# Kernel optimization log

Hardware: AMD Instinct MI355X
Metric: run time of the kernel (lower is better)

## Reference

```python
import jax, jax.numpy as jnp
import numpy as np

RANGES = {"measure": 256, "beat": 16, "position": 128, "duration": 128, "pitch": 256,
          "instrument": 129, "velocity": 128, "key_sign": 24, "time_sign": 48, "tempo": 49}
R_TOTAL = sum(RANGES.values())  # 1162
NUMERATORS = jnp.array([1, 2, 3, 4, 5, 6, 7, 8, 9, 10, 12, 16], dtype=jnp.int32)
TOT_NUM = 12
NEG = jnp.float32(-1e9)


def _prefix_gather(x, axis=1):
    # value at position i becomes the cumulative value at index min(i+1, S-1):
    # reproduces the tf mask `range(S) <= idx+1` (prefix up to i+1 inclusive).
    S = x.shape[axis]
    idx = jnp.minimum(jnp.arange(S) + 1, S - 1)
    return jnp.take(x, idx, axis=axis)


def _present_mask(song, dtype_id, feat, R):
    # occ[b,i,v] = True iff some token j<=i+1 has type dtype_id and song[b,j,feat]==v
    # (vectorized form of tensor_scatter_nd_max over a prefix, via one-hot + cummax)
    match = song[..., 0] == dtype_id                       # [B,S]
    onehot = (song[..., feat][..., None] == jnp.arange(R)) & match[..., None]
    cum = jax.lax.cummax(onehot.astype(jnp.int32), axis=1)
    return _prefix_gather(cum, 1).astype(bool)             # [B,S,R]


def _has_any(song, dtype_id):
    match = (song[..., 0] == dtype_id).astype(jnp.int32)
    return _prefix_gather(jax.lax.cummax(match, axis=1), 1).astype(bool)  # [B,S]


def _last_value(song, dtype_id, feat):
    # song[b, argmax_j(match*j) , feat] over the prefix j<=i+1; tf argmax of all
    # zeros returns 0, reproduced by where(match, j, 0) + cummax.
    match = song[..., 0] == dtype_id
    j = jnp.arange(song.shape[1])
    last_idx = _prefix_gather(jax.lax.cummax(jnp.where(match, j, 0), axis=1), 1)
    return jnp.take_along_axis(song[..., feat], last_idx, axis=1)  # [B,S]


def _forward(song, chosen_type, scores):
    B, S, _ = song.shape
    Rm, Rb = RANGES["measure"], RANGES["beat"]
    ar_m = jnp.arange(RANGES["measure"]); ar_b = jnp.arange(RANGES["beat"])
    ar_p = jnp.arange(RANGES["position"])
    ar_ks = jnp.arange(RANGES["key_sign"]); ar_ts = jnp.arange(RANGES["time_sign"])
    ar_tp = jnp.arange(RANGES["tempo"])
    t = chosen_type[..., None]  # [B,S,1]

    inst_present = _present_mask(song, 1, 6, RANGES["instrument"])  # [B,S,129]
    has_inst = inst_present.any(-1, keepdims=True)

    last_ks = _last_value(song, 4, 8);  oh_ks = last_ks[..., None] == ar_ks
    last_ts = _last_value(song, 5, 9);  oh_ts = last_ts[..., None] == ar_ts
    last_tp = _last_value(song, 6, 10); oh_tp = last_tp[..., None] == ar_tp
    has_ks = _has_any(song, 4)[..., None]
    has_ts = _has_any(song, 5)[..., None]

    # ---- chosen_type == 3 (note-like token) ----
    min_measure = song[..., 1]
    pred_m = jnp.argmax(scores[..., :Rm], axis=-1).astype(jnp.int32)
    c1 = pred_m == min_measure
    min_beat = jnp.where(c1, song[..., 2], 0)
    pred_b = jnp.argmax(scores[..., Rm:Rm + Rb], axis=-1).astype(jnp.int32)
    c2 = c1 & (pred_b == min_beat)
    min_pos = jnp.where(c2, song[..., 3], 0)
    max_beat = NUMERATORS[jnp.mod(last_ts, TOT_NUM)]  # get_max_beat_from_time_sign
    m3 = ar_m >= min_measure[..., None]
    b3 = (ar_b >= min_beat[..., None]) & (ar_b < max_beat[..., None])
    p3 = ar_p >= min_pos[..., None]

    # ---- chosen_type == 1 (instrument): forbid already-present instruments ----
    inst1 = jnp.where(has_inst, ~inst_present, True)

    # ---- chosen_type in 4..6 (key_sign / time_sign / tempo) ----
    min_m46 = jnp.where((song[..., 2] == 0) & (song[..., 3] == 0),
                        song[..., 1], song[..., 1] + 1)
    m46 = ar_m >= min_m46[..., None]
    ks4 = jnp.where(has_ks, ~oh_ks, True)
    ts5 = jnp.where(has_ts, ~oh_ts, True)
    tp6 = ~oh_tp

    is3 = t == 3
    measure_mask = jnp.where(is3, m3, jnp.where((t >= 4) & (t <= 6), m46, True))
    beat_mask = jnp.where(is3, b3, True)
    position_mask = jnp.where(is3, p3, True)
    duration_mask = jnp.ones((B, S, RANGES["duration"]), bool)
    pitch_mask = jnp.ones((B, S, RANGES["pitch"]), bool)
    instrument_mask = jnp.where(is3, inst_present, jnp.where(t == 1, inst1, True))
    velocity_mask = jnp.ones((B, S, RANGES["velocity"]), bool)
    key_sign_mask = jnp.where(is3, oh_ks, jnp.where(t == 4, ks4, True))
    time_sign_mask = jnp.where(is3, oh_ts, jnp.where(t == 5, ts5, True))
    tempo_mask = jnp.where(is3, oh_tp, jnp.where(t == 6, tp6, True))

    mask = jnp.concatenate([measure_mask, beat_mask, position_mask, duration_mask,
                            pitch_mask, instrument_mask, velocity_mask,
                            key_sign_mask, time_sign_mask, tempo_mask], axis=-1)
    return jnp.where(mask, scores, NEG)  # masked logits [B,S,R_TOTAL]


def setup_inputs() -> dict:
    key = jax.random.key(0)
    k_song, k_type, k_scores = jax.random.split(key, 3)
    B, S = 8, 2047  # SEQ_LEN-1 with SEQ_LEN=2048
    col_max = [8, RANGES["measure"], RANGES["beat"], RANGES["position"],
               RANGES["duration"], RANGES["pitch"], RANGES["instrument"],
               RANGES["velocity"], RANGES["key_sign"], RANGES["time_sign"],
               RANGES["tempo"]]
    kcols = jax.random.split(k_song, 11)
    song = jnp.stack([jax.random.randint(kcols[c], (B, S), 0, col_max[c],
                                         dtype=jnp.int32) for c in range(11)], axis=-1)
    chosen_type = jax.random.randint(k_type, (B, S), 0, 8, dtype=jnp.int32)
    scores = jax.random.normal(k_scores, (B, S, R_TOTAL), dtype=jnp.float32)
    return {"song": song, "chosen_type": chosen_type, "scores": scores}


def reference(song, chosen_type, scores):
    return _forward(song, chosen_type, scores)
```

## Files before the change

kernel.cpp:

```cpp
#include <hip/hip_runtime.h>
#include <cstdint>
#include <cstddef>

#define S_LEN 2047
#define BATCH 8
#define R_TOT 1162
#define NCHUNK 8
#define NEGV (-1e9f)

#define CARRY_OFF 393024

__device__ __constant__ int d_numerators[12] = {1, 2, 3, 4, 5, 6, 7, 8, 9, 10, 12, 16};

__global__ __launch_bounds__(256) void scan_local(const int* __restrict__ song,
                                                  unsigned* __restrict__ local) {
    const int b = blockIdx.x >> 3;
    const int c = blockIdx.x & 7;
    const int tid = threadIdx.x;
    const int j = c * 256 + tid;
    __shared__ unsigned lds_f[3][256];
    __shared__ unsigned lds_inst[5][256];
    const unsigned HAS = 1u << 16;
    const long base = (long)b * S_LEN;

    unsigned e_f[3] = {0, 0, 0};
    unsigned e_inst[5] = {0, 0, 0, 0, 0};
    if (j < S_LEN) {
        const int* rj = song + (base + j) * 11;
        const int type = rj[0];
        if (type == 4)      e_f[0] = HAS | (unsigned)rj[8];
        else if (type == 5) e_f[1] = HAS | (unsigned)rj[9];
        else if (type == 6) e_f[2] = HAS | (unsigned)rj[10];
        else if (type == 1) { const int v = rj[6]; e_inst[v >> 5] = 1u << (v & 31); }
    }
#pragma unroll
    for (int w = 0; w < 3; w++) lds_f[w][tid] = e_f[w];
#pragma unroll
    for (int w = 0; w < 5; w++) lds_inst[w][tid] = e_inst[w];
    __syncthreads();

    for (int off = 1; off < 256; off <<= 1) {
        unsigned p_f[3] = {0, 0, 0};
        unsigned p_inst[5] = {0, 0, 0, 0, 0};
        if (tid >= off) {
#pragma unroll
            for (int w = 0; w < 3; w++) p_f[w] = lds_f[w][tid - off];
#pragma unroll
            for (int w = 0; w < 5; w++) p_inst[w] = lds_inst[w][tid - off];
        }
        __syncthreads();
        if (tid >= off) {
#pragma unroll
            for (int w = 0; w < 3; w++) {
                if (!(e_f[w] & HAS)) e_f[w] = p_f[w];
                lds_f[w][tid] = e_f[w];
            }
#pragma unroll
            for (int w = 0; w < 5; w++) {
                e_inst[w] |= p_inst[w];
                lds_inst[w][tid] = e_inst[w];
            }
        }
        __syncthreads();
    }

    if (j < S_LEN) {
        const unsigned w0 =
            (e_f[0] & 0xFFu) | ((e_f[1] & 0xFFu) << 8) | ((e_f[2] & 0xFFu) << 16) |
            (((e_f[0] >> 16) & 1u) << 24) | (((e_f[1] >> 16) & 1u) << 25) |
            (((e_f[2] >> 16) & 1u) << 26);
        unsigned* sp = local + (size_t)(base + j) * 6;
        sp[0] = w0;
#pragma unroll
        for (int w = 0; w < 5; w++) sp[1 + w] = e_inst[w];
    }
}

__global__ __launch_bounds__(64) void scan_carry(const int* __restrict__ song,
                                                 const unsigned* __restrict__ local,
                                                 unsigned* __restrict__ carry) {
    const int b = threadIdx.x;
    if (b >= BATCH) return;
    const int* r0 = song + (size_t)b * S_LEN * 11;
    unsigned cks = (unsigned)r0[8], cts = (unsigned)r0[9], ctp = (unsigned)r0[10];
    unsigned chas = 0;
    unsigned cinst[5] = {0, 0, 0, 0, 0};
    for (int c = 0; c < NCHUNK; c++) {
        unsigned* cp = carry + ((size_t)b * NCHUNK + c) * 6;
        cp[0] = (cks & 0xFFu) | ((cts & 0xFFu) << 8) | ((ctp & 0xFFu) << 16) | (chas << 24);
#pragma unroll
        for (int w = 0; w < 5; w++) cp[1 + w] = cinst[w];
        const int pos = min((c + 1) * 256, S_LEN) - 1;
        const unsigned* lp = local + ((size_t)b * S_LEN + pos) * 6;
        const unsigned a0 = lp[0];
        if ((a0 >> 24) & 1u) cks = a0 & 0xFFu;
        if ((a0 >> 25) & 1u) cts = (a0 >> 8) & 0xFFu;
        if ((a0 >> 26) & 1u) ctp = (a0 >> 16) & 0xFFu;
        chas |= (a0 >> 24) & 7u;
#pragma unroll
        for (int w = 0; w < 5; w++) cinst[w] |= lp[1 + w];
    }
}

__global__ __launch_bounds__(256) void mask_kernel(const int* __restrict__ song,
                                                   const int* __restrict__ ctype,
                                                   const float* __restrict__ scores,
                                                   const unsigned* __restrict__ local,
                                                   const unsigned* __restrict__ carry,
                                                   float* __restrict__ out) {
    const int row = blockIdx.x;
    const int tid = threadIdx.x;
    const int b = row / S_LEN;
    const int i = row - b * S_LEN;

    __shared__ float s_val[128];
    __shared__ int   s_idx[128];
    __shared__ float sb_val[8];
    __shared__ int   sb_idx[8];
    __shared__ int   s_info[10];
    __shared__ int   f_info[17];

    const size_t rbase = (size_t)row * R_TOT;
    const float2* s2 = (const float2*)(scores + rbase);
    float2* o2 = (float2*)(out + rbase);

    const int t0 = ctype[row];

    const float2 r0 = s2[tid];
    const float2 r1 = s2[tid + 256];
    float2 r2 = make_float2(0.f, 0.f);
    if (tid < 69) r2 = s2[tid + 512];

    if (t0 == 0 || t0 == 2 || t0 == 7) {
        o2[tid] = r0;
        o2[tid + 256] = r1;
        if (tid < 69) o2[tid + 512] = r2;
        return;
    }

    if (tid < 128) {
        const bool sec = (r0.y > r0.x);
        s_val[tid] = sec ? r0.y : r0.x;
        s_idx[tid] = 2 * tid + (sec ? 1 : 0);
    } else if (tid < 136) {
        const bool sec = (r0.y > r0.x);
        sb_val[tid - 128] = sec ? r0.y : r0.x;
        sb_idx[tid - 128] = (2 * tid - 256) + (sec ? 1 : 0);
    } else if (tid < 142) {
        const int w = tid - 136;
        const int e = min(i + 1, S_LEN - 1);
        const unsigned lw = local[((size_t)b * S_LEN + e) * 6 + w];
        const unsigned cw = carry[((size_t)b * NCHUNK + (e >> 8)) * 6 + w];
        unsigned v;
        if (w == 0) {
            const unsigned ks = ((lw >> 24) & 1u) ? (lw & 0xFFu) : (cw & 0xFFu);
            const unsigned ts = ((lw >> 25) & 1u) ? ((lw >> 8) & 0xFFu) : ((cw >> 8) & 0xFFu);
            const unsigned tp = ((lw >> 26) & 1u) ? ((lw >> 16) & 0xFFu) : ((cw >> 16) & 0xFFu);
            const unsigned hks = ((lw >> 24) | (cw >> 24)) & 1u;
            const unsigned hts = ((lw >> 25) | (cw >> 25)) & 1u;
            v = ks | (ts << 8) | (tp << 16) | (hks << 24) | (hts << 25);
        } else {
            v = lw | cw;
        }
        s_info[w] = (int)v;
    } else if (tid < 146) {
        const int* srow = song + (size_t)row * 11;
        if (tid == 142) s_info[6] = srow[1];
        if (tid == 143) s_info[7] = srow[2];
        if (tid == 144) s_info[8] = srow[3];
        if (tid == 145) s_info[9] = ctype[row];
    }
    __syncthreads();

    if (t0 == 3) {
        for (int s = 64; s > 0; s >>= 1) {
            if (tid < s) {
                if (s_val[tid + s] > s_val[tid]) {
                    s_val[tid] = s_val[tid + s];
                    s_idx[tid] = s_idx[tid + s];
                }
            }
            __syncthreads();
        }
    }

    if (tid == 0) {
        int pred_m = -1, pred_b = -1;
        if (t0 == 3) {
            pred_m = s_idx[0];
            float bv = sb_val[0];
            pred_b = sb_idx[0];
#pragma unroll
            for (int q = 1; q < 8; q++) {
                if (sb_val[q] > bv) { bv = sb_val[q]; pred_b = sb_idx[q]; }
            }
        }
        const unsigned pack = (unsigned)s_info[0];
        const int song1 = s_info[6], song2 = s_info[7], song3 = s_info[8];
        const int t = s_info[9];
        const bool c1 = (pred_m == song1);
        const int min_beat = c1 ? song2 : 0;
        const bool c2 = c1 && (pred_b == min_beat);
        const int min_pos = c2 ? song3 : 0;
        const int last_ks = pack & 0xFF;
        const int last_ts = (pack >> 8) & 0xFF;
        const int last_tp = (pack >> 16) & 0xFF;
        f_info[0] = t;
        f_info[1] = song1;
        f_info[2] = min_beat;
        f_info[3] = min_pos;
        f_info[4] = (song2 == 0 && song3 == 0) ? song1 : song1 + 1;
        f_info[5] = d_numerators[last_ts % 12];
        f_info[6] = last_ks;
        f_info[7] = last_ts;
        f_info[8] = last_tp;
        f_info[9]  = (int)((pack >> 24) & 1u);
        f_info[10] = (int)((pack >> 25) & 1u);
        const unsigned u = (unsigned)s_info[1] | (unsigned)s_info[2] | (unsigned)s_info[3] |
                           (unsigned)s_info[4] | (unsigned)s_info[5];
        f_info[11] = (u != 0u);
        f_info[12] = s_info[1]; f_info[13] = s_info[2]; f_info[14] = s_info[3];
        f_info[15] = s_info[4]; f_info[16] = s_info[5];
    }
    __syncthreads();

    const int t = f_info[0];
    const int min_measure = f_info[1], min_beat = f_info[2], min_pos = f_info[3];
    const int min_m46 = f_info[4], max_beat = f_info[5];
    const int last_ks = f_info[6], last_ts = f_info[7], last_tp = f_info[8];
    const bool has_ks = f_info[9] != 0, has_ts = f_info[10] != 0, has_inst = f_info[11] != 0;
    unsigned inst[5];
#pragma unroll
    for (int w = 0; w < 5; w++) inst[w] = (unsigned)f_info[12 + w];
    const bool is3 = (t == 3);
    const bool is46 = (t >= 4) && (t <= 6);

    auto maskf = [&](int col) -> bool {
        if (col < 256) {
            if (is3) return col >= min_measure;
            if (is46) return col >= min_m46;
            return true;
        } else if (col < 272) {
            if (!is3) return true;
            const int v = col - 256;
            return (v >= min_beat) && (v < max_beat);
        } else if (col < 400) {
            return is3 ? ((col - 272) >= min_pos) : true;
        } else if (col < 784) {
            return true;
        } else if (col < 913) {
            const int v = col - 784;
            const bool pres = ((inst[v >> 5] >> (v & 31)) & 1u) != 0u;
            if (is3) return pres;
            if (t == 1) return has_inst ? !pres : true;
            return true;
        } else if (col < 1041) {
            return true;
        } else if (col < 1065) {
            const int v = col - 1041;
            if (is3) return v == last_ks;
            if (t == 4) return has_ks ? (v != last_ks) : true;
            return true;
        } else if (col < 1113) {
            const int v = col - 1065;
            if (is3) return v == last_ts;
            if (t == 5) return has_ts ? (v != last_ts) : true;
            return true;
        } else {
            const int v = col - 1113;
            if (is3) return v == last_tp;
            if (t == 6) return v != last_tp;
            return true;
        }
    };

    float2 w;
    int c = 2 * tid;
    w.x = maskf(c)     ? r0.x : NEGV;
    w.y = maskf(c + 1) ? r0.y : NEGV;
    o2[tid] = w;

    c = 512 + 2 * tid;
    w.x = maskf(c)     ? r1.x : NEGV;
    w.y = maskf(c + 1) ? r1.y : NEGV;
    o2[tid + 256] = w;

    if (tid < 69) {
        c = 1024 + 2 * tid;
        w.x = maskf(c)     ? r2.x : NEGV;
        w.y = maskf(c + 1) ? r2.y : NEGV;
        o2[tid + 512] = w;
    }
}

extern "C" void kernel_launch(void* const* d_in, const int* in_sizes, int n_in,
                              void* d_out, int out_size, void* d_ws, size_t ws_size,
                              hipStream_t stream) {
    const int* song = (const int*)d_in[0];
    const int* ctype = (const int*)d_in[1];
    const float* scores = (const float*)d_in[2];
    float* out = (float*)d_out;
    unsigned* local = (unsigned*)d_ws;
    unsigned* carry = (unsigned*)((char*)d_ws + CARRY_OFF);

    scan_local<<<BATCH * NCHUNK, 256, 0, stream>>>(song, local);
    scan_carry<<<1, 64, 0, stream>>>(song, local, carry);
    mask_kernel<<<BATCH * S_LEN, 256, 0, stream>>>(song, ctype, scores, local, carry, out);
}
```

Before: 146.7 us.

## Split masking into per-row bitmask kernel and flat float4 streaming kernel

The single per-row mask kernel becomes two kernels. A row_state kernel computes a 37-word per-row bitmask into workspace, reading scores only for type-3 rows. A grid-stride stream_mask kernel then applies that bitmask to the whole scores tensor with coalesced float4 loads and stores. The goal is to replace the awkward 1162-wide per-row float2 access with a uniform streaming pass. The cost is an extra kernel launch, a bitmask write and read, and per-element division and gathers into the bitmask table. If the workspace is too small, the old kernel is used instead.

Result: slower. 172.2 us (+17.4%).

```diff
diff --git a/kernel.cpp b/kernel.cpp
--- a/kernel.cpp
+++ b/kernel.cpp
@@ -7,8 +7,13 @@
 #define R_TOT 1162
 #define NCHUNK 8
 #define NEGV (-1e9f)
+#define NROWS (BATCH * S_LEN)
+#define N4 4757228
+#define MWORDS 37
 
 #define CARRY_OFF 393024
+#define MTAB_OFF  394560
+#define WS_NEED   (MTAB_OFF + (size_t)NROWS * MWORDS * 4)
 
 __device__ __constant__ int d_numerators[12] = {1, 2, 3, 4, 5, 6, 7, 8, 9, 10, 12, 16};
 
@@ -102,12 +107,12 @@
     }
 }
 
-__global__ __launch_bounds__(256) void mask_kernel(const int* __restrict__ song,
-                                                   const int* __restrict__ ctype,
-                                                   const float* __restrict__ scores,
-                                                   const unsigned* __restrict__ local,
-                                                   const unsigned* __restrict__ carry,
-                                                   float* __restrict__ out) {
+__global__ __launch_bounds__(256) void row_state(const int* __restrict__ song,
+                                                 const int* __restrict__ ctype,
+                                                 const float* __restrict__ scores,
+                                                 const unsigned* __restrict__ local,
+                                                 const unsigned* __restrict__ carry,
+                                                 unsigned* __restrict__ mtab) {
     const int row = blockIdx.x;
     const int tid = threadIdx.x;
     const int b = row / S_LEN;
@@ -120,33 +125,30 @@
     __shared__ int   s_info[10];
     __shared__ int   f_info[17];
 
+    const int t0 = ctype[row];
+    unsigned* mrow = mtab + (size_t)row * MWORDS;
+
+    if (t0 == 0 || t0 == 2 || t0 == 7) {
+        if (tid < MWORDS) mrow[tid] = 0xFFFFFFFFu;
+        return;
+    }
+
     const size_t rbase = (size_t)row * R_TOT;
     const float2* s2 = (const float2*)(scores + rbase);
-    float2* o2 = (float2*)(out + rbase);
-
-    const int t0 = ctype[row];
-
-    const float2 r0 = s2[tid];
-    const float2 r1 = s2[tid + 256];
-    float2 r2 = make_float2(0.f, 0.f);
-    if (tid < 69) r2 = s2[tid + 512];
-
-    if (t0 == 0 || t0 == 2 || t0 == 7) {
-        o2[tid] = r0;
-        o2[tid + 256] = r1;
-        if (tid < 69) o2[tid + 512] = r2;
-        return;
-    }
-
-    if (tid < 128) {
-        const bool sec = (r0.y > r0.x);
-        s_val[tid] = sec ? r0.y : r0.x;
-        s_idx[tid] = 2 * tid + (sec ? 1 : 0);
-    } else if (tid < 136) {
-        const bool sec = (r0.y > r0.x);
-        sb_val[tid - 128] = sec ? r0.y : r0.x;
-        sb_idx[tid - 128] = (2 * tid - 256) + (sec ? 1 : 0);
-    } else if (tid < 142) {
+
+    if (t0 == 3 && tid < 136) {
+        const float2 r0 = s2[tid];
+        if (tid < 128) {
+            const bool sec = (r0.y > r0.x);
+            s_val[tid] = sec ? r0.y : r0.x;
+            s_idx[tid] = 2 * tid + (sec ? 1 : 0);
+        } else {
+            const bool sec = (r0.y > r0.x);
+            sb_val[tid - 128] = sec ? r0.y : r0.x;
+            sb_idx[tid - 128] = (2 * tid - 256) + (sec ? 1 : 0);
+        }
+    }
+    if (tid >= 136 && tid < 142) {
         const int w = tid - 136;
         const int e = min(i + 1, S_LEN - 1);
         const unsigned lw = local[((size_t)b * S_LEN + e) * 6 + w];
@@ -163,7 +165,7 @@
             v = lw | cw;
         }
         s_info[w] = (int)v;
-    } else if (tid < 146) {
+    } else if (tid >= 142 && tid < 146) {
         const int* srow = song + (size_t)row * 11;
         if (tid == 142) s_info[6] = srow[1];
         if (tid == 143) s_info[7] = srow[2];
@@ -274,6 +276,225 @@
         }
     };
 
+    const int wv = tid >> 6;
+    const int lane = tid & 63;
+#pragma unroll
+    for (int it = 0; it < 5; it++) {
+        const int colb = it * 256 + wv * 64;
+        const int col = colb + lane;
+        const bool pred = (col < R_TOT) ? maskf(col) : false;
+        const unsigned long long m = __ballot(pred);
+        const int w_idx = colb >> 5;
+        if (lane == 0 && w_idx < MWORDS) mrow[w_idx] = (unsigned)m;
+        if (lane == 1 && w_idx + 1 < MWORDS) mrow[w_idx + 1] = (unsigned)(m >> 32);
+    }
+}
+
+__global__ __launch_bounds__(256) void stream_mask(const float* __restrict__ scores,
+                                                   const unsigned* __restrict__ mtab,
+                                                   float* __restrict__ out) {
+    const int stride = gridDim.x * 256;
+    for (int f = blockIdx.x * 256 + threadIdx.x; f < N4; f += stride) {
+        const unsigned fe = (unsigned)f * 4u;
+        unsigned row = fe / 1162u;
+        unsigned col = fe - row * 1162u;
+        const float4 v = ((const float4*)scores)[f];
+        float4 w;
+        {
+            const unsigned bits = mtab[row * MWORDS + (col >> 5)];
+            w.x = ((bits >> (col & 31u)) & 1u) ? v.x : NEGV;
+            if (++col == 1162u) { col = 0u; ++row; }
+        }
+        {
+            const unsigned bits = mtab[row * MWORDS + (col >> 5)];
+            w.y = ((bits >> (col & 31u)) & 1u) ? v.y : NEGV;
+            if (++col == 1162u) { col = 0u; ++row; }
+        }
+        {
+            const unsigned bits = mtab[row * MWORDS + (col >> 5)];
+            w.z = ((bits >> (col & 31u)) & 1u) ? v.z : NEGV;
+            if (++col == 1162u) { col = 0u; ++row; }
+        }
+        {
+            const unsigned bits = mtab[row * MWORDS + (col >> 5)];
+            w.w = ((bits >> (col & 31u)) & 1u) ? v.w : NEGV;
+        }
+        ((float4*)out)[f] = w;
+    }
+}
+
+__global__ __launch_bounds__(256) void mask_kernel(const int* __restrict__ song,
+                                                   const int* __restrict__ ctype,
+                                                   const float* __restrict__ scores,
+                                                   const unsigned* __restrict__ local,
+                                                   const unsigned* __restrict__ carry,
+                                                   float* __restrict__ out) {
+    const int row = blockIdx.x;
+    const int tid = threadIdx.x;
+    const int b = row / S_LEN;
+    const int i = row - b * S_LEN;
+
+    __shared__ float s_val[128];
+    __shared__ int   s_idx[128];
+    __shared__ float sb_val[8];
+    __shared__ int   sb_idx[8];
+    __shared__ int   s_info[10];
+    __shared__ int   f_info[17];
+
+    const size_t rbase = (size_t)row * R_TOT;
+    const float2* s2 = (const float2*)(scores + rbase);
+    float2* o2 = (float2*)(out + rbase);
+
+    const int t0 = ctype[row];
+
+    const float2 r0 = s2[tid];
+    const float2 r1 = s2[tid + 256];
+    float2 r2 = make_float2(0.f, 0.f);
+    if (tid < 69) r2 = s2[tid + 512];
+
+    if (t0 == 0 || t0 == 2 || t0 == 7) {
+        o2[tid] = r0;
+        o2[tid + 256] = r1;
+        if (tid < 69) o2[tid + 512] = r2;
+        return;
+    }
+
+    if (tid < 128) {
+        const bool sec = (r0.y > r0.x);
+        s_val[tid] = sec ? r0.y : r0.x;
+        s_idx[tid] = 2 * tid + (sec ? 1 : 0);
+    } else if (tid < 136) {
+        const bool sec = (r0.y > r0.x);
+        sb_val[tid - 128] = sec ? r0.y : r0.x;
+        sb_idx[tid - 128] = (2 * tid - 256) + (sec ? 1 : 0);
+    } else if (tid < 142) {
+        const int w = tid - 136;
+        const int e = min(i + 1, S_LEN - 1);
+        const unsigned lw = local[((size_t)b * S_LEN + e) * 6 + w];
+        const unsigned cw = carry[((size_t)b * NCHUNK + (e >> 8)) * 6 + w];
+        unsigned v;
+        if (w == 0) {
+            const unsigned ks = ((lw >> 24) & 1u) ? (lw & 0xFFu) : (cw & 0xFFu);
+            const unsigned ts = ((lw >> 25) & 1u) ? ((lw >> 8) & 0xFFu) : ((cw >> 8) & 0xFFu);
+            const unsigned tp = ((lw >> 26) & 1u) ? ((lw >> 16) & 0xFFu) : ((cw >> 16) & 0xFFu);
+            const unsigned hks = ((lw >> 24) | (cw >> 24)) & 1u;
+            const unsigned hts = ((lw >> 25) | (cw >> 25)) & 1u;
+            v = ks | (ts << 8) | (tp << 16) | (hks << 24) | (hts << 25);
+        } else {
+            v = lw | cw;
+        }
+        s_info[w] = (int)v;
+    } else if (tid < 146) {
+        const int* srow = song + (size_t)row * 11;
+        if (tid == 142) s_info[6] = srow[1];
+        if (tid == 143) s_info[7] = srow[2];
+        if (tid == 144) s_info[8] = srow[3];
+        if (tid == 145) s_info[9] = ctype[row];
+    }
+    __syncthreads();
+
+    if (t0 == 3) {
+        for (int s = 64; s > 0; s >>= 1) {
+            if (tid < s) {
+                if (s_val[tid + s] > s_val[tid]) {
+                    s_val[tid] = s_val[tid + s];
+                    s_idx[tid] = s_idx[tid + s];
+                }
+            }
+            __syncthreads();
+        }
+    }
+
+    if (tid == 0) {
+        int pred_m = -1, pred_b = -1;
+        if (t0 == 3) {
+            pred_m = s_idx[0];
+            float bv = sb_val[0];
+            pred_b = sb_idx[0];
+#pragma unroll
+            for (int q = 1; q < 8; q++) {
+                if (sb_val[q] > bv) { bv = sb_val[q]; pred_b = sb_idx[q]; }
+            }
+        }
+        const unsigned pack = (unsigned)s_info[0];
+        const int song1 = s_info[6], song2 = s_info[7], song3 = s_info[8];
+        const int t = s_info[9];
+        const bool c1 = (pred_m == song1);
+        const int min_beat = c1 ? song2 : 0;
+        const bool c2 = c1 && (pred_b == min_beat);
+        const int min_pos = c2 ? song3 : 0;
+        const int last_ks = pack & 0xFF;
+        const int last_ts = (pack >> 8) & 0xFF;
+        const int last_tp = (pack >> 16) & 0xFF;
+        f_info[0] = t;
+        f_info[1] = song1;
+        f_info[2] = min_beat;
+        f_info[3] = min_pos;
+        f_info[4] = (song2 == 0 && song3 == 0) ? song1 : song1 + 1;
+        f_info[5] = d_numerators[last_ts % 12];
+        f_info[6] = last_ks;
+        f_info[7] = last_ts;
+        f_info[8] = last_tp;
+        f_info[9]  = (int)((pack >> 24) & 1u);
+        f_info[10] = (int)((pack >> 25) & 1u);
+        const unsigned u = (unsigned)s_info[1] | (unsigned)s_info[2] | (unsigned)s_info[3] |
+                           (unsigned)s_info[4] | (unsigned)s_info[5];
+        f_info[11] = (u != 0u);
+        f_info[12] = s_info[1]; f_info[13] = s_info[2]; f_info[14] = s_info[3];
+        f_info[15] = s_info[4]; f_info[16] = s_info[5];
+    }
+    __syncthreads();
+
+    const int t = f_info[0];
+    const int min_measure = f_info[1], min_beat = f_info[2], min_pos = f_info[3];
+    const int min_m46 = f_info[4], max_beat = f_info[5];
+    const int last_ks = f_info[6], last_ts = f_info[7], last_tp = f_info[8];
+    const bool has_ks = f_info[9] != 0, has_ts = f_info[10] != 0, has_inst = f_info[11] != 0;
+    unsigned inst[5];
+#pragma unroll
+    for (int w = 0; w < 5; w++) inst[w] = (unsigned)f_info[12 + w];
+    const bool is3 = (t == 3);
+    const bool is46 = (t >= 4) && (t <= 6);
+
+    auto maskf = [&](int col) -> bool {
+        if (col < 256) {
+            if (is3) return col >= min_measure;
+            if (is46) return col >= min_m46;
+            return true;
+        } else if (col < 272) {
+            if (!is3) return true;
+            const int v = col - 256;
+            return (v >= min_beat) && (v < max_beat);
+        } else if (col < 400) {
+            return is3 ? ((col - 272) >= min_pos) : true;
+        } else if (col < 784) {
+            return true;
+        } else if (col < 913) {
+            const int v = col - 784;
+            const bool pres = ((inst[v >> 5] >> (v & 31)) & 1u) != 0u;
+            if (is3) return pres;
+            if (t == 1) return has_inst ? !pres : true;
+            return true;
+        } else if (col < 1041) {
+            return true;
+        } else if (col < 1065) {
+            const int v = col - 1041;
+            if (is3) return v == last_ks;
+            if (t == 4) return has_ks ? (v != last_ks) : true;
+            return true;
+        } else if (col < 1113) {
+            const int v = col - 1065;
+            if (is3) return v == last_ts;
+            if (t == 5) return has_ts ? (v != last_ts) : true;
+            return true;
+        } else {
+            const int v = col - 1113;
+            if (is3) return v == last_tp;
+            if (t == 6) return v != last_tp;
+            return true;
+        }
+    };
+
     float2 w;
     int c = 2 * tid;
     w.x = maskf(c)     ? r0.x : NEGV;
@@ -305,5 +526,12 @@
 
     scan_local<<<BATCH * NCHUNK, 256, 0, stream>>>(song, local);
     scan_carry<<<1, 64, 0, stream>>>(song, local, carry);
-    mask_kernel<<<BATCH * S_LEN, 256, 0, stream>>>(song, ctype, scores, local, carry, out);
+
+    if (ws_size >= WS_NEED) {
+        unsigned* mtab = (unsigned*)((char*)d_ws + MTAB_OFF);
+        row_state<<<NROWS, 256, 0, stream>>>(song, ctype, scores, local, carry, mtab);
+        stream_mask<<<2048, 256, 0, stream>>>(scores, mtab, out);
+    } else {
+        mask_kernel<<<NROWS, 256, 0, stream>>>(song, ctype, scores, local, carry, out);
+    }
 }
```

## Convert mask kernel to grid-stride loop with next-row score prefetch

Applied to the files above, without the earlier changes.

The mask kernel now launches a fixed grid of 2048 blocks instead of one block per row. Each block loops over rows with a stride of the grid size and loads the next row's scores into registers before working on the current row. The aim is to overlap global loads with mask computation and to cut block launch overhead. In exchange, fewer blocks are in flight for the memory system, more registers are live per thread, and an extra barrier runs at the end of each masked row so shared memory can be reused safely.

After: 157.6 us. +7.4%, slower.

```diff
diff --git a/kernel.cpp b/kernel.cpp
--- a/kernel.cpp
+++ b/kernel.cpp
@@ -7,6 +7,8 @@
 #define R_TOT 1162
 #define NCHUNK 8
 #define NEGV (-1e9f)
+#define NROWS (BATCH * S_LEN)
+#define MGRID 2048
 
 #define CARRY_OFF 393024
 
@@ -108,10 +110,7 @@
                                                    const unsigned* __restrict__ local,
                                                    const unsigned* __restrict__ carry,
                                                    float* __restrict__ out) {
-    const int row = blockIdx.x;
     const int tid = threadIdx.x;
-    const int b = row / S_LEN;
-    const int i = row - b * S_LEN;
 
     __shared__ float s_val[128];
     __shared__ int   s_idx[128];
@@ -120,176 +119,197 @@
     __shared__ int   s_info[10];
     __shared__ int   f_info[17];
 
-    const size_t rbase = (size_t)row * R_TOT;
-    const float2* s2 = (const float2*)(scores + rbase);
-    float2* o2 = (float2*)(out + rbase);
-
-    const int t0 = ctype[row];
-
-    const float2 r0 = s2[tid];
-    const float2 r1 = s2[tid + 256];
-    float2 r2 = make_float2(0.f, 0.f);
-    if (tid < 69) r2 = s2[tid + 512];
-
-    if (t0 == 0 || t0 == 2 || t0 == 7) {
-        o2[tid] = r0;
-        o2[tid + 256] = r1;
-        if (tid < 69) o2[tid + 512] = r2;
-        return;
-    }
-
-    if (tid < 128) {
-        const bool sec = (r0.y > r0.x);
-        s_val[tid] = sec ? r0.y : r0.x;
-        s_idx[tid] = 2 * tid + (sec ? 1 : 0);
-    } else if (tid < 136) {
-        const bool sec = (r0.y > r0.x);
-        sb_val[tid - 128] = sec ? r0.y : r0.x;
-        sb_idx[tid - 128] = (2 * tid - 256) + (sec ? 1 : 0);
-    } else if (tid < 142) {
-        const int w = tid - 136;
-        const int e = min(i + 1, S_LEN - 1);
-        const unsigned lw = local[((size_t)b * S_LEN + e) * 6 + w];
-        const unsigned cw = carry[((size_t)b * NCHUNK + (e >> 8)) * 6 + w];
-        unsigned v;
-        if (w == 0) {
-            const unsigned ks = ((lw >> 24) & 1u) ? (lw & 0xFFu) : (cw & 0xFFu);
-            const unsigned ts = ((lw >> 25) & 1u) ? ((lw >> 8) & 0xFFu) : ((cw >> 8) & 0xFFu);
-            const unsigned tp = ((lw >> 26) & 1u) ? ((lw >> 16) & 0xFFu) : ((cw >> 16) & 0xFFu);
-            const unsigned hks = ((lw >> 24) | (cw >> 24)) & 1u;
-            const unsigned hts = ((lw >> 25) | (cw >> 25)) & 1u;
-            v = ks | (ts << 8) | (tp << 16) | (hks << 24) | (hts << 25);
+    int row = blockIdx.x;
+
+    float2 r0, r1, r2;
+    {
+        const float2* s2 = (const float2*)(scores + (size_t)row * R_TOT);
+        r0 = s2[tid];
+        r1 = s2[tid + 256];
+        r2 = make_float2(0.f, 0.f);
+        if (tid < 69) r2 = s2[tid + 512];
+    }
+
+    while (row < NROWS) {
+        const int nrow = row + MGRID;
+        const size_t rbase = (size_t)row * R_TOT;
+        float2* o2 = (float2*)(out + rbase);
+        const int b = row / S_LEN;
+        const int i = row - b * S_LEN;
+        const int t0 = ctype[row];
+
+        float2 n0 = make_float2(0.f, 0.f), n1 = n0, n2 = n0;
+        if (nrow < NROWS) {
+            const float2* ns2 = (const float2*)(scores + (size_t)nrow * R_TOT);
+            n0 = ns2[tid];
+            n1 = ns2[tid + 256];
+            if (tid < 69) n2 = ns2[tid + 512];
+        }
+
+        if (t0 == 0 || t0 == 2 || t0 == 7) {
+            o2[tid] = r0;
+            o2[tid + 256] = r1;
+            if (tid < 69) o2[tid + 512] = r2;
         } else {
-            v = lw | cw;
-        }
-        s_info[w] = (int)v;
-    } else if (tid < 146) {
-        const int* srow = song + (size_t)row * 11;
-        if (tid == 142) s_info[6] = srow[1];
-        if (tid == 143) s_info[7] = srow[2];
-        if (tid == 144) s_info[8] = srow[3];
-        if (tid == 145) s_info[9] = ctype[row];
-    }
-    __syncthreads();
-
-    if (t0 == 3) {
-        for (int s = 64; s > 0; s >>= 1) {
-            if (tid < s) {
-                if (s_val[tid + s] > s_val[tid]) {
-                    s_val[tid] = s_val[tid + s];
-                    s_idx[tid] = s_idx[tid + s];
+            if (tid < 128) {
+                const bool sec = (r0.y > r0.x);
+                s_val[tid] = sec ? r0.y : r0.x;
+                s_idx[tid] = 2 * tid + (sec ? 1 : 0);
+            } else if (tid < 136) {
+                const bool sec = (r0.y > r0.x);
+                sb_val[tid - 128] = sec ? r0.y : r0.x;
+                sb_idx[tid - 128] = (2 * tid - 256) + (sec ? 1 : 0);
+            } else if (tid < 142) {
+                const int w = tid - 136;
+                const int e = min(i + 1, S_LEN - 1);
+                const unsigned lw = local[((size_t)b * S_LEN + e) * 6 + w];
+                const unsigned cw = carry[((size_t)b * NCHUNK + (e >> 8)) * 6 + w];
+                unsigned v;
+                if (w == 0) {
+                    const unsigned ks = ((lw >> 24) & 1u) ? (lw & 0xFFu) : (cw & 0xFFu);
+                    const unsigned ts = ((lw >> 25) & 1u) ? ((lw >> 8) & 0xFFu) : ((cw >> 8) & 0xFFu);
+                    const unsigned tp = ((lw >> 26) & 1u) ? ((lw >> 16) & 0xFFu) : ((cw >> 16) & 0xFFu);
+                    const unsigned hks = ((lw >> 24) | (cw >> 24)) & 1u;
+                    const unsigned hts = ((lw >> 25) | (cw >> 25)) & 1u;
+                    v = ks | (ts << 8) | (tp << 16) | (hks << 24) | (hts << 25);
+                } else {
+                    v = lw | cw;
                 }
-            }
+                s_info[w] = (int)v;
+            } else if (tid < 146) {
+                const int* srow = song + (size_t)row * 11;
+                if (tid == 142) s_info[6] = srow[1];
+                if (tid == 143) s_info[7] = srow[2];
+                if (tid == 144) s_info[8] = srow[3];
+                if (tid == 145) s_info[9] = ctype[row];
+            }
+            __syncthreads();
+
+            if (t0 == 3) {
+                for (int s = 64; s > 0; s >>= 1) {
+                    if (tid < s) {
+                        if (s_val[tid + s] > s_val[tid]) {
+                            s_val[tid] = s_val[tid + s];
+                            s_idx[tid] = s_idx[tid + s];
+                        }
+                    }
+                    __syncthreads();
+                }
+            }
+
+            if (tid == 0) {
+                int pred_m = -1, pred_b = -1;
+                if (t0 == 3) {
+                    pred_m = s_idx[0];
+                    float bv = sb_val[0];
+                    pred_b = sb_idx[0];
+#pragma unroll
+                    for (int q = 1; q < 8; q++) {
+                        if (sb_val[q] > bv) { bv = sb_val[q]; pred_b = sb_idx[q]; }
+                    }
+                }
+                const unsigned pack = (unsigned)s_info[0];
+                const int song1 = s_info[6], song2 = s_info[7], song3 = s_info[8];
+                const int t = s_info[9];
+                const bool c1 = (pred_m == song1);
+                const int min_beat = c1 ? song2 : 0;
+                const bool c2 = c1 && (pred_b == min_beat);
+                const int min_pos = c2 ? song3 : 0;
+                const int last_ks = pack & 0xFF;
+                const int last_ts = (pack >> 8) & 0xFF;
+                const int last_tp = (pack >> 16) & 0xFF;
+                f_info[0] = t;
+                f_info[1] = song1;
+                f_info[2] = min_beat;
+                f_info[3] = min_pos;
+                f_info[4] = (song2 == 0 && song3 == 0) ? song1 : song1 + 1;
+                f_info[5] = d_numerators[last_ts % 12];
+                f_info[6] = last_ks;
+                f_info[7] = last_ts;
+                f_info[8] = last_tp;
+                f_info[9]  = (int)((pack >> 24) & 1u);
+                f_info[10] = (int)((pack >> 25) & 1u);
+                const unsigned u = (unsigned)s_info[1] | (unsigned)s_info[2] | (unsigned)s_info[3] |
+                                   (unsigned)s_info[4] | (unsigned)s_info[5];
+                f_info[11] = (u != 0u);
+                f_info[12] = s_info[1]; f_info[13] = s_info[2]; f_info[14] = s_info[3];
+                f_info[15] = s_info[4]; f_info[16] = s_info[5];
+            }
+            __syncthreads();
+
+            const int t = f_info[0];
+            const int min_measure = f_info[1], min_beat = f_info[2], min_pos = f_info[3];
+            const int min_m46 = f_info[4], max_beat = f_info[5];
+            const int last_ks = f_info[6], last_ts = f_info[7], last_tp = f_info[8];
+            const bool has_ks = f_info[9] != 0, has_ts = f_info[10] != 0, has_inst = f_info[11] != 0;
+            unsigned inst[5];
+#pragma unroll
+            for (int w = 0; w < 5; w++) inst[w] = (unsigned)f_info[12 + w];
+            const bool is3 = (t == 3);
+            const bool is46 = (t >= 4) && (t <= 6);
+
+            auto maskf = [&](int col) -> bool {
+                if (col < 256) {
+                    if (is3) return col >= min_measure;
+                    if (is46) return col >= min_m46;
+                    return true;
+                } else if (col < 272) {
+                    if (!is3) return true;
+                    const int v = col - 256;
+                    return (v >= min_beat) && (v < max_beat);
+                } else if (col < 400) {
+                    return is3 ? ((col - 272) >= min_pos) : true;
+                } else if (col < 784) {
+                    return true;
+                } else if (col < 913) {
+                    const int v = col - 784;
+                    const bool pres = ((inst[v >> 5] >> (v & 31)) & 1u) != 0u;
+                    if (is3) return pres;
+                    if (t == 1) return has_inst ? !pres : true;
+                    return true;
+                } else if (col < 1041) {
+                    return true;
+                } else if (col < 1065) {
+                    const int v = col - 1041;
+                    if (is3) return v == last_ks;
+                    if (t == 4) return has_ks ? (v != last_ks) : true;
+                    return true;
+                } else if (col < 1113) {
+                    const int v = col - 1065;
+                    if (is3) return v == last_ts;
+                    if (t == 5) return has_ts ? (v != last_ts) : true;
+                    return true;
+                } else {
+                    const int v = col - 1113;
+                    if (is3) return v == last_tp;
+                    if (t == 6) return v != last_tp;
+                    return true;
+                }
+            };
+
+            float2 w;
+            int c = 2 * tid;
+            w.x = maskf(c)     ? r0.x : NEGV;
+            w.y = maskf(c + 1) ? r0.y : NEGV;
+            o2[tid] = w;
+
+            c = 512 + 2 * tid;
+            w.x = maskf(c)     ? r1.x : NEGV;
+            w.y = maskf(c + 1) ? r1.y : NEGV;
+            o2[tid + 256] = w;
+
+            if (tid < 69) {
+                c = 1024 + 2 * tid;
+                w.x = maskf(c)     ? r2.x : NEGV;
+                w.y = maskf(c + 1) ? r2.y : NEGV;
+                o2[tid + 512] = w;
+            }
+
             __syncthreads();
         }
-    }
-
-    if (tid == 0) {
-        int pred_m = -1, pred_b = -1;
-        if (t0 == 3) {
-            pred_m = s_idx[0];
-            float bv = sb_val[0];
-            pred_b = sb_idx[0];
-#pragma unroll
-            for (int q = 1; q < 8; q++) {
-                if (sb_val[q] > bv) { bv = sb_val[q]; pred_b = sb_idx[q]; }
-            }
-        }
-        const unsigned pack = (unsigned)s_info[0];
-        const int song1 = s_info[6], song2 = s_info[7], song3 = s_info[8];
-        const int t = s_info[9];
-        const bool c1 = (pred_m == song1);
-        const int min_beat = c1 ? song2 : 0;
-        const bool c2 = c1 && (pred_b == min_beat);
-        const int min_pos = c2 ? song3 : 0;
-        const int last_ks = pack & 0xFF;
-        const int last_ts = (pack >> 8) & 0xFF;
-        const int last_tp = (pack >> 16) & 0xFF;
-        f_info[0] = t;
-        f_info[1] = song1;
-        f_info[2] = min_beat;
-        f_info[3] = min_pos;
-        f_info[4] = (song2 == 0 && song3 == 0) ? song1 : song1 + 1;
-        f_info[5] = d_numerators[last_ts % 12];
-        f_info[6] = last_ks;
-        f_info[7] = last_ts;
-        f_info[8] = last_tp;
-        f_info[9]  = (int)((pack >> 24) & 1u);
-        f_info[10] = (int)((pack >> 25) & 1u);
-        const unsigned u = (unsigned)s_info[1] | (unsigned)s_info[2] | (unsigned)s_info[3] |
-                           (unsigned)s_info[4] | (unsigned)s_info[5];
-        f_info[11] = (u != 0u);
-        f_info[12] = s_info[1]; f_info[13] = s_info[2]; f_info[14] = s_info[3];
-        f_info[15] = s_info[4]; f_info[16] = s_info[5];
-    }
-    __syncthreads();
-
-    const int t = f_info[0];
-    const int min_measure = f_info[1], min_beat = f_info[2], min_pos = f_info[3];
-    const int min_m46 = f_info[4], max_beat = f_info[5];
-    const int last_ks = f_info[6], last_ts = f_info[7], last_tp = f_info[8];
-    const bool has_ks = f_info[9] != 0, has_ts = f_info[10] != 0, has_inst = f_info[11] != 0;
-    unsigned inst[5];
-#pragma unroll
-    for (int w = 0; w < 5; w++) inst[w] = (unsigned)f_info[12 + w];
-    const bool is3 = (t == 3);
-    const bool is46 = (t >= 4) && (t <= 6);
-
-    auto maskf = [&](int col) -> bool {
-        if (col < 256) {
-            if (is3) return col >= min_measure;
-            if (is46) return col >= min_m46;
-            return true;
-        } else if (col < 272) {
-            if (!is3) return true;
-            const int v = col - 256;
-            return (v >= min_beat) && (v < max_beat);
-        } else if (col < 400) {
-            return is3 ? ((col - 272) >= min_pos) : true;
-        } else if (col < 784) {
-            return true;
-        } else if (col < 913) {
-            const int v = col - 784;
-            const bool pres = ((inst[v >> 5] >> (v & 31)) & 1u) != 0u;
-            if (is3) return pres;
-            if (t == 1) return has_inst ? !pres : true;
-            return true;
-        } else if (col < 1041) {
-            return true;
-        } else if (col < 1065) {
-            const int v = col - 1041;
-            if (is3) return v == last_ks;
-            if (t == 4) return has_ks ? (v != last_ks) : true;
-            return true;
-        } else if (col < 1113) {
-            const int v = col - 1065;
-            if (is3) return v == last_ts;
-            if (t == 5) return has_ts ? (v != last_ts) : true;
-            return true;
-        } else {
-            const int v = col - 1113;
-            if (is3) return v == last_tp;
-            if (t == 6) return v != last_tp;
-            return true;
-        }
-    };
-
-    float2 w;
-    int c = 2 * tid;
-    w.x = maskf(c)     ? r0.x : NEGV;
-    w.y = maskf(c + 1) ? r0.y : NEGV;
-    o2[tid] = w;
-
-    c = 512 + 2 * tid;
-    w.x = maskf(c)     ? r1.x : NEGV;
-    w.y = maskf(c + 1) ? r1.y : NEGV;
-    o2[tid + 256] = w;
-
-    if (tid < 69) {
-        c = 1024 + 2 * tid;
-        w.x = maskf(c)     ? r2.x : NEGV;
-        w.y = maskf(c + 1) ? r2.y : NEGV;
-        o2[tid + 512] = w;
+
+        r0 = n0; r1 = n1; r2 = n2;
+        row = nrow;
     }
 }
 
@@ -305,5 +325,5 @@
 
     scan_local<<<BATCH * NCHUNK, 256, 0, stream>>>(song, local);
     scan_carry<<<1, 64, 0, stream>>>(song, local, carry);
-    mask_kernel<<<BATCH * S_LEN, 256, 0, stream>>>(song, ctype, scores, local, carry, out);
+    mask_kernel<<<MGRID, 256, 0, stream>>>(song, ctype, scores, local, carry, out);
 }
```
